# Kernel optimization log

Measured on AMD Instinct MI355X. Metric: run time of the kernel, lower is better.

The kernel has to match this reference:

```python
import jax, jax.numpy as jnp
import numpy as np

N_HEADS = 16
HEAD_DIM = 64
SEQ_LEN = 2048
BATCH = 1


def alibi_slopes(n_heads):
    start = 2.0 ** (-8.0 / n_heads)
    return jnp.asarray([start * start ** i for i in range(n_heads)], dtype=jnp.float32)


def setup_inputs() -> dict:
    key = jax.random.key(0)
    kq, kk, kv = jax.random.split(key, 3)
    shape = (BATCH, N_HEADS, SEQ_LEN, HEAD_DIM)
    return {
        "q": jax.random.normal(kq, shape, dtype=jnp.float32),
        "k": jax.random.normal(kk, shape, dtype=jnp.float32),
        "v": jax.random.normal(kv, shape, dtype=jnp.float32),
    }


def reference(q, k, v):
    # q,k,v: [B,H,S,D]
    seq_len = q.shape[2]
    head_dim = q.shape[3]
    scale = 1.0 / np.sqrt(head_dim).astype(np.float32)
    # scores: [B,H,S,S]
    scores = jnp.einsum("bhsd,bhtd->bhst", q, k) * scale
    pos = jnp.arange(seq_len)
    # distances[i, j] = j - i  (pos.unsqueeze(0) - pos.unsqueeze(1))
    distances = (pos[None, :] - pos[:, None]).astype(jnp.float32)  # [S,S]
    slopes = alibi_slopes(q.shape[1])  # [H]
    alibi = slopes[:, None, None] * distances[None, :, :]  # [H,S,S]
    scores = scores + alibi[None]
    attn = jax.nn.softmax(scores, axis=-1)
    return jnp.einsum("bhst,bhtd->bhsd", attn, v)
```

## Files before the change

### kernel.cpp

```cpp
#include <hip/hip_runtime.h>
#include <hip/hip_bf16.h>
#include <stdint.h>
#include <math.h>

#define N_HEADS 16
#define HEAD_DIM 64
#define SEQ_LEN 2048
#define KVBLK 64
#define NT 16
#define NTILE_TOT (SEQ_LEN / 32)

typedef __bf16 bf16x8 __attribute__((ext_vector_type(8)));
typedef __bf16 bf16x4 __attribute__((ext_vector_type(4)));
typedef short  s16x4  __attribute__((ext_vector_type(4)));
typedef float  f32x4  __attribute__((ext_vector_type(4)));
typedef unsigned int u32x4 __attribute__((ext_vector_type(4)));

#if __has_builtin(__builtin_amdgcn_mfma_f32_16x16x16bf16_1k)
#define HAVE_MFMA16 1
#else
#define HAVE_MFMA16 0
#endif

#if __has_builtin(__builtin_amdgcn_global_load_lds)
#define HAVE_GLL 1
#define GLL16(gsrc, ldst)                                                     \
    __builtin_amdgcn_global_load_lds(                                         \
        (const __attribute__((address_space(1))) void*)(gsrc),                \
        (__attribute__((address_space(3))) void*)(ldst), 16, 0, 0)
#else
#define HAVE_GLL 0
#endif

static __device__ __forceinline__ unsigned pkbf(float a, float b) {
    union { __bf16 h[2]; unsigned u; } t;
    t.h[0] = (__bf16)a; t.h[1] = (__bf16)b;
    return t.u;
}

static __device__ __forceinline__ int vpos(int k) {
#if HAVE_MFMA16
    return ((k & 12) << 2) + ((k & 16) >> 1) + ((k & 3) << 1);
#else
    return k * 2;
#endif
}

__global__ __launch_bounds__(256)
void prep_kernel(const float* __restrict__ k,
                 const float* __restrict__ v,
                 char* __restrict__ kimg,
                 char* __restrict__ vtimg,
                 float* __restrict__ tilemax) {
    const int ts  = blockIdx.x;
    const int h   = blockIdx.y;
    const int tid = threadIdx.x;
    const int s0  = ts * 32;
    const size_t blk = ((size_t)h * NTILE_TOT + ts) * 4096;

    __shared__ float redmax[4];

    const int krow = tid >> 3;
    const int kcol = (tid & 7) * 8;
    const float* ks = k + ((size_t)h * SEQ_LEN + s0 + krow) * HEAD_DIM + kcol;
    f32x4 a = *(const f32x4*)ks;
    f32x4 b = *(const f32x4*)(ks + 4);
    bf16x8 kb;
    float pn = 0.0f;
    #pragma unroll
    for (int i = 0; i < 4; ++i) {
        kb[i] = (__bf16)a[i]; kb[4 + i] = (__bf16)b[i];
        pn += a[i] * a[i] + b[i] * b[i];
    }
    *(bf16x8*)(kimg + blk + krow * 128 + ((kcol * 2) ^ ((krow & 7) << 4))) = kb;

    pn += __shfl_xor(pn, 1);
    pn += __shfl_xor(pn, 2);
    pn += __shfl_xor(pn, 4);
    float wmax = pn;
    wmax = fmaxf(wmax, __shfl_xor(wmax, 8));
    wmax = fmaxf(wmax, __shfl_xor(wmax, 16));
    wmax = fmaxf(wmax, __shfl_xor(wmax, 32));
    if ((tid & 63) == 0) redmax[tid >> 6] = wmax;

    const int vc = tid & 63;
    const int vr = (tid >> 6) * 8;
    const float* vs = v + ((size_t)h * SEQ_LEN + s0 + vr) * HEAD_DIM + vc;
    bf16x4 vb0, vb1;
    #pragma unroll
    for (int j = 0; j < 4; ++j) {
        vb0[j] = (__bf16)vs[(size_t)j * HEAD_DIM];
        vb1[j] = (__bf16)vs[(size_t)(4 + j) * HEAD_DIM];
    }
    const int swzV = (vc & 7) << 4;
    *(bf16x4*)(vtimg + blk + ((vc * 64 + vpos(vr))     ^ swzV)) = vb0;
    *(bf16x4*)(vtimg + blk + ((vc * 64 + vpos(vr + 4)) ^ swzV)) = vb1;

    __syncthreads();
    if (tid == 0) {
        tilemax[h * NTILE_TOT + ts] = fmaxf(fmaxf(redmax[0], redmax[1]),
                                            fmaxf(redmax[2], redmax[3]));
    }
}

template <bool IMG>
__global__ __launch_bounds__(512, 2)
void attn_alibi_kernel(const float* __restrict__ q,
                       const float* __restrict__ k,
                       const float* __restrict__ v,
                       float* __restrict__ out,
                       const char* __restrict__ kimg,
                       const char* __restrict__ vtimg,
                       const float* __restrict__ tilemax) {
    const int tid  = threadIdx.x;
    const int wave = tid >> 6;
    const int lane = tid & 63;
    const int col  = lane & 15;
    const int g    = lane >> 4;
    const int half = wave >> 2;
    const int w4   = wave & 3;

    const int h      = blockIdx.y;
    const int qbase  = blockIdx.x * 64 + w4 * 16;
    const int kstart = half * (NT * KVBLK);

    const float* qh = q + (size_t)h * SEQ_LEN * HEAD_DIM;
    const float* kh = k + (size_t)h * SEQ_LEN * HEAD_DIM;
    const float* vh = v + (size_t)h * SEQ_LEN * HEAD_DIM;

    __shared__ alignas(16) char smem[65536];
    char* kbase  = smem + half * 16384;
    char* vtbase = smem + 32768 + half * 16384;

    const float LOG2E  = 1.4426950408889634f;
    const float scale2 = 0.125f * LOG2E;
    const float slope  = exp2f(-0.5f * (float)(h + 1));
    const float slope2 = slope * LOG2E;

    bf16x8 qf[2];
    float qn2 = 0.0f;
    {
        const float* qr = qh + (size_t)(qbase + col) * HEAD_DIM + g * 8;
        #pragma unroll
        for (int c = 0; c < 2; ++c)
            #pragma unroll
            for (int b = 0; b < 8; ++b) {
                float x = qr[c * 32 + b];
                qn2 += x * x;
                qf[c][b] = (__bf16)x;
            }
    }
    qn2 += __shfl_xor(qn2, 16);
    qn2 += __shfl_xor(qn2, 32);

    float knmax;
    if constexpr (IMG) {
        float tm = tilemax[h * NTILE_TOT + lane];
        tm = fmaxf(tm, __shfl_xor(tm, 1));
        tm = fmaxf(tm, __shfl_xor(tm, 2));
        tm = fmaxf(tm, __shfl_xor(tm, 4));
        tm = fmaxf(tm, __shfl_xor(tm, 8));
        tm = fmaxf(tm, __shfl_xor(tm, 16));
        tm = fmaxf(tm, __shfl_xor(tm, 32));
        knmax = sqrtf(tm);
    } else {
        knmax = 16.0f;
    }
    const int   kend = kstart + NT * KVBLK;
    const float m = slope2 * (float)(kend - 1 - (qbase + col))
                  + scale2 * sqrtf(qn2) * knmax * 1.05f;

    float cbm[4][4];
    #pragma unroll
    for (int i = 0; i < 4; ++i)
        #pragma unroll
        for (int r = 0; r < 4; ++r)
            cbm[i][r] = slope2 * (float)(i * 16 + g * 4 + r - (qbase + col)) - m;

    float l = 0.0f;
    f32x4 acc[4];
    #pragma unroll
    for (int dt = 0; dt < 4; ++dt) acc[dt] = (f32x4)0.0f;

    const int hid  = tid & 255;
    const int krow = hid >> 3;
    const int kcol = (hid & 7) * 8;
    const int vc   = hid & 63;
    const int vr   = (hid >> 6) * 8;

    const char* kis = nullptr; const char* vis = nullptr;
    const float* ksrc = nullptr; const float* vsrc = nullptr;
    char* kdst = nullptr; char* vtdst0 = nullptr; char* vtdst1 = nullptr;
    if constexpr (IMG) {
        const size_t base = ((size_t)h * NTILE_TOT + half * (NTILE_TOT / 2)) * 4096
                          + hid * 16;
        kis = kimg + base;  vis = vtimg + base;
#if HAVE_GLL
        kdst   = kbase + w4 * 1024;
        vtdst0 = vtbase + w4 * 1024;
#else
        kdst   = kbase + hid * 16;
        vtdst0 = vtbase + hid * 16;
#endif
    } else {
        ksrc  = kh + (size_t)(kstart + krow) * HEAD_DIM + kcol;
        kdst  = kbase + krow * 128 + ((kcol * 2) ^ ((krow & 7) << 4));
        vsrc  = vh + (size_t)(kstart + vr) * HEAD_DIM + vc;
        const int swzV = (vc & 7) << 4;
        vtdst0 = vtbase + ((vc * 64 + vpos(vr))     ^ swzV);
        vtdst1 = vtbase + ((vc * 64 + vpos(vr + 4)) ^ swzV);
    }

    f32x4 kreg[2], vreg[2];
    f32x4 kr[2][2];
    float vv[2][8];

    if constexpr (IMG) {
#if HAVE_GLL
        #pragma unroll
        for (int sb = 0; sb < 2; ++sb) {
            GLL16(kis + sb * 4096, kdst   + sb * 4096);
            GLL16(vis + sb * 4096, vtdst0 + sb * 4096);
        }
#else
        #pragma unroll
        for (int sb = 0; sb < 2; ++sb) {
            kreg[sb] = *(const f32x4*)(kis + sb * 4096);
            vreg[sb] = *(const f32x4*)(vis + sb * 4096);
            *(f32x4*)(kdst   + sb * 4096) = kreg[sb];
            *(f32x4*)(vtdst0 + sb * 4096) = vreg[sb];
        }
#endif
    } else {
        #pragma unroll
        for (int sb = 0; sb < 2; ++sb) {
            const float* ks = ksrc + (size_t)(sb * 32) * HEAD_DIM;
            const float* vs = vsrc + (size_t)(sb * 32) * HEAD_DIM;
            kr[sb][0] = *(const f32x4*)(ks);
            kr[sb][1] = *(const f32x4*)(ks + 4);
            #pragma unroll
            for (int j = 0; j < 8; ++j) vv[sb][j] = vs[(size_t)j * HEAD_DIM];
            bf16x8 kb16;
            bf16x4 vb0, vb1;
            #pragma unroll
            for (int b = 0; b < 4; ++b) {
                kb16[b] = (__bf16)kr[sb][0][b]; kb16[4 + b] = (__bf16)kr[sb][1][b];
                vb0[b] = (__bf16)vv[sb][b];     vb1[b] = (__bf16)vv[sb][4 + b];
            }
            *(bf16x8*)(kdst   + sb * 4096) = kb16;
            *(bf16x4*)(vtdst0 + sb * 4096) = vb0;
            *(bf16x4*)(vtdst1 + sb * 4096) = vb1;
        }
    }
    __syncthreads();

    for (int t = 0; t < NT; ++t) {
        const int kb  = kstart + t * KVBLK;
        const int buf = t & 1;
        const char* kbuf  = kbase + buf * 8192;
        const char* vtbuf = vtbase + buf * 8192;

#if HAVE_GLL
        if (IMG && t + 1 < NT) {
            const int nb = (t + 1) & 1;
            #pragma unroll
            for (int sb = 0; sb < 2; ++sb) {
                GLL16(kis + (size_t)((t + 1) * 2 + sb) * 4096,
                      kdst + nb * 8192 + sb * 4096);
                GLL16(vis + (size_t)((t + 1) * 2 + sb) * 4096,
                      vtdst0 + nb * 8192 + sb * 4096);
            }
        }
#endif

        f32x4 sacc[4];
        #pragma unroll
        for (int i = 0; i < 4; ++i) sacc[i] = (f32x4)0.0f;
        __builtin_amdgcn_s_setprio(1);
        #pragma unroll
        for (int sb = 0; sb < 2; ++sb) {
            #pragma unroll
            for (int jt = 0; jt < 2; ++jt) {
                const int row = jt * 16 + col;
                const int i   = sb * 2 + jt;
                #pragma unroll
                for (int c = 0; c < 2; ++c) {
                    bf16x8 kf = *(const bf16x8*)(kbuf + sb * 4096 + row * 128
                                                 + ((c * 64 + g * 16) ^ ((row & 7) << 4)));
                    sacc[i] = __builtin_amdgcn_mfma_f32_16x16x32_bf16(kf, qf[c], sacc[i], 0, 0, 0);
                }
            }
        }
        __builtin_amdgcn_s_setprio(0);

        if (t + 1 < NT) {
            if constexpr (IMG) {
#if !HAVE_GLL
                #pragma unroll
                for (int sb = 0; sb < 2; ++sb) {
                    kreg[sb] = *(const f32x4*)(kis + (size_t)((t + 1) * 2 + sb) * 4096);
                    vreg[sb] = *(const f32x4*)(vis + (size_t)((t + 1) * 2 + sb) * 4096);
                }
#endif
            } else {
                #pragma unroll
                for (int sb = 0; sb < 2; ++sb) {
                    const float* ks = ksrc + (size_t)((t + 1) * 64 + sb * 32) * HEAD_DIM;
                    const float* vs = vsrc + (size_t)((t + 1) * 64 + sb * 32) * HEAD_DIM;
                    kr[sb][0] = *(const f32x4*)(ks);
                    kr[sb][1] = *(const f32x4*)(ks + 4);
                    #pragma unroll
                    for (int j = 0; j < 8; ++j) vv[sb][j] = vs[(size_t)j * HEAD_DIM];
                }
            }
        }

        const float skb = slope2 * (float)kb;
        float p[4][4], y = 0.0f;
        #pragma unroll
        for (int i = 0; i < 4; ++i)
            #pragma unroll
            for (int r = 0; r < 4; ++r) {
                float sv = sacc[i][r] * scale2 + (cbm[i][r] + skb);
                p[i][r] = __builtin_amdgcn_exp2f(sv);
                y += p[i][r];
            }
        l += y;

#if HAVE_MFMA16
        s16x4 pb[4];
        #pragma unroll
        for (int i = 0; i < 4; ++i) {
            bf16x4 pf;
            #pragma unroll
            for (int b = 0; b < 4; ++b) pf[b] = (__bf16)p[i][b];
            pb[i] = __builtin_bit_cast(s16x4, pf);
        }
        __builtin_amdgcn_s_setprio(1);
        #pragma unroll
        for (int dt = 0; dt < 4; ++dt) {
            const int vrow = dt * 16 + col;
            const int off  = (vrow * 64 + g * 16) ^ ((vrow & 7) << 4);
            #pragma unroll
            for (int sb = 0; sb < 2; ++sb) {
                bf16x8 vf = *(const bf16x8*)(vtbuf + sb * 4096 + off);
                bf16x4 vlo = __builtin_shufflevector(vf, vf, 0, 1, 2, 3);
                bf16x4 vhi = __builtin_shufflevector(vf, vf, 4, 5, 6, 7);
                acc[dt] = __builtin_amdgcn_mfma_f32_16x16x16bf16_1k(
                    __builtin_bit_cast(s16x4, vlo), pb[sb * 2 + 0], acc[dt], 0, 0, 0);
                acc[dt] = __builtin_amdgcn_mfma_f32_16x16x16bf16_1k(
                    __builtin_bit_cast(s16x4, vhi), pb[sb * 2 + 1], acc[dt], 0, 0, 0);
            }
        }
        __builtin_amdgcn_s_setprio(0);
#else
        #pragma unroll
        for (int sb = 0; sb < 2; ++sb) {
            unsigned pk00 = pkbf(p[sb * 2][0],     p[sb * 2][1]);
            unsigned pk01 = pkbf(p[sb * 2][2],     p[sb * 2][3]);
            unsigned pk10 = pkbf(p[sb * 2 + 1][0], p[sb * 2 + 1][1]);
            unsigned pk11 = pkbf(p[sb * 2 + 1][2], p[sb * 2 + 1][3]);
            const int srcA = col + ((g & 1) << 5);
            const int srcB = srcA + 16;
            unsigned a00 = __shfl(pk00, srcA), a01 = __shfl(pk01, srcA);
            unsigned a10 = __shfl(pk10, srcA), a11 = __shfl(pk11, srcA);
            unsigned b00 = __shfl(pk00, srcB), b01 = __shfl(pk01, srcB);
            unsigned b10 = __shfl(pk10, srcB), b11 = __shfl(pk11, srcB);
            const bool hi = g >= 2;
            u32x4 pu;
            pu[0] = hi ? a10 : a00;
            pu[1] = hi ? a11 : a01;
            pu[2] = hi ? b10 : b00;
            pu[3] = hi ? b11 : b01;
            bf16x8 pf = __builtin_bit_cast(bf16x8, pu);
            #pragma unroll
            for (int dt = 0; dt < 4; ++dt) {
                const int vrow = dt * 16 + col;
                bf16x8 vf = *(const bf16x8*)(vtbuf + sb * 4096
                                + ((vrow * 64 + g * 16) ^ ((vrow & 7) << 4)));
                acc[dt] = __builtin_amdgcn_mfma_f32_16x16x32_bf16(vf, pf, acc[dt], 0, 0, 0);
            }
        }
#endif

        if (t + 1 < NT) {
            const int nb = (t + 1) & 1;
            if constexpr (IMG) {
#if !HAVE_GLL
                #pragma unroll
                for (int sb = 0; sb < 2; ++sb) {
                    *(f32x4*)(kdst   + nb * 8192 + sb * 4096) = kreg[sb];
                    *(f32x4*)(vtdst0 + nb * 8192 + sb * 4096) = vreg[sb];
                }
#endif
            } else {
                #pragma unroll
                for (int sb = 0; sb < 2; ++sb) {
                    bf16x8 kb16;
                    bf16x4 vb0, vb1;
                    #pragma unroll
                    for (int b = 0; b < 4; ++b) {
                        kb16[b] = (__bf16)kr[sb][0][b]; kb16[4 + b] = (__bf16)kr[sb][1][b];
                        vb0[b] = (__bf16)vv[sb][b];     vb1[b] = (__bf16)vv[sb][4 + b];
                    }
                    *(bf16x8*)(kdst   + nb * 8192 + sb * 4096) = kb16;
                    *(bf16x4*)(vtdst0 + nb * 8192 + sb * 4096) = vb0;
                    *(bf16x4*)(vtdst1 + nb * 8192 + sb * 4096) = vb1;
                }
            }
        }
        __syncthreads();
    }

    l += __shfl_xor(l, 16);
    l += __shfl_xor(l, 32);

    float* eacc = (float*)smem;
    float* eml  = (float*)(smem + 16384);

    if (half == 1) {
        #pragma unroll
        for (int dt = 0; dt < 4; ++dt)
            *(f32x4*)(eacc + w4 * 1024 + col * 64 + dt * 16 + g * 4) = acc[dt];
        if (g == 0) {
            eml[(w4 * 16 + col) * 2 + 0] = m;
            eml[(w4 * 16 + col) * 2 + 1] = l;
        }
    }
    __syncthreads();
    if (half == 0) {
        float m2 = eml[(w4 * 16 + col) * 2 + 0];
        float l2 = eml[(w4 * 16 + col) * 2 + 1];
        float mm = fmaxf(m, m2);
        float a1 = __builtin_amdgcn_exp2f(m - mm);
        float a2 = __builtin_amdgcn_exp2f(m2 - mm);
        float inv = 1.0f / (l * a1 + l2 * a2);
        float* orow = out + ((size_t)h * SEQ_LEN + qbase + col) * HEAD_DIM;
        #pragma unroll
        for (int dt = 0; dt < 4; ++dt) {
            f32x4 o2 = *(const f32x4*)(eacc + w4 * 1024 + col * 64 + dt * 16 + g * 4);
            *(f32x4*)(orow + dt * 16 + g * 4) = (acc[dt] * a1 + o2 * a2) * inv;
        }
    }
}

extern "C" void kernel_launch(void* const* d_in, const int* in_sizes, int n_in,
                              void* d_out, int out_size, void* d_ws, size_t ws_size,
                              hipStream_t stream) {
    const float* q = (const float*)d_in[0];
    const float* k = (const float*)d_in[1];
    const float* v = (const float*)d_in[2];
    float* out = (float*)d_out;

    const size_t imgBytes = (size_t)N_HEADS * NTILE_TOT * 4096;
    const size_t need = 2 * imgBytes + N_HEADS * NTILE_TOT * sizeof(float);

    dim3 grid(SEQ_LEN / 64, N_HEADS, 1);
    if (ws_size >= need) {
        char* kimg     = (char*)d_ws;
        char* vtimg    = kimg + imgBytes;
        float* tilemax = (float*)(vtimg + imgBytes);
        prep_kernel<<<dim3(NTILE_TOT, N_HEADS, 1), dim3(256, 1, 1), 0, stream>>>(
            k, v, kimg, vtimg, tilemax);
        attn_alibi_kernel<true><<<grid, dim3(512, 1, 1), 0, stream>>>(
            q, k, v, out, kimg, vtimg, tilemax);
    } else {
        attn_alibi_kernel<false><<<grid, dim3(512, 1, 1), 0, stream>>>(
            q, k, v, out, nullptr, nullptr, nullptr);
    }
}
```

Baseline: 43.39 us.

## Split KV four ways with 32x32 MFMA and skip ALiBi-negligible key tiles

Restructures the attention kernel so each block's eight waves split the key range into four quarters of 512 keys. Each wave handles 32 queries using 32x32 bf16 MFMAs, and the four partial results are merged through shared memory at the end. Key tiles far enough from the sequence end that the ALiBi bias drives exp2 below about 2^-160 relative to the running bound are skipped per head, which removes much of the work for steep-slope heads. The softmax scale is folded into Q, the V image layout is simplified, and launch bounds are raised to target more blocks per CU. The costs are uneven load across quarters, a four-way merge epilogue, and reliance on the precomputed max bound for the tile-skip rule to stay correct.

```diff
diff --git a/kernel.cpp b/kernel.cpp
--- a/kernel.cpp
+++ b/kernel.cpp
@@ -6,20 +6,19 @@
 #define N_HEADS 16
 #define HEAD_DIM 64
 #define SEQ_LEN 2048
-#define KVBLK 64
-#define NT 16
-#define NTILE_TOT (SEQ_LEN / 32)
+#define NTILE_TOT 64
+#define NTQ 16
 
 typedef __bf16 bf16x8 __attribute__((ext_vector_type(8)));
 typedef __bf16 bf16x4 __attribute__((ext_vector_type(4)));
 typedef short  s16x4  __attribute__((ext_vector_type(4)));
 typedef float  f32x4  __attribute__((ext_vector_type(4)));
-typedef unsigned int u32x4 __attribute__((ext_vector_type(4)));
-
-#if __has_builtin(__builtin_amdgcn_mfma_f32_16x16x16bf16_1k)
-#define HAVE_MFMA16 1
+typedef float  f32x16 __attribute__((ext_vector_type(16)));
+
+#if __has_builtin(__builtin_amdgcn_mfma_f32_32x32x8bf16_1k)
+#define HAVE_K8 1
 #else
-#define HAVE_MFMA16 0
+#define HAVE_K8 0
 #endif
 
 #if __has_builtin(__builtin_amdgcn_global_load_lds)
@@ -36,14 +35,6 @@
     union { __bf16 h[2]; unsigned u; } t;
     t.h[0] = (__bf16)a; t.h[1] = (__bf16)b;
     return t.u;
-}
-
-static __device__ __forceinline__ int vpos(int k) {
-#if HAVE_MFMA16
-    return ((k & 12) << 2) + ((k & 16) >> 1) + ((k & 3) << 1);
-#else
-    return k * 2;
-#endif
 }
 
 __global__ __launch_bounds__(256)
@@ -86,15 +77,10 @@
     const int vc = tid & 63;
     const int vr = (tid >> 6) * 8;
     const float* vs = v + ((size_t)h * SEQ_LEN + s0 + vr) * HEAD_DIM + vc;
-    bf16x4 vb0, vb1;
+    bf16x8 vb;
     #pragma unroll
-    for (int j = 0; j < 4; ++j) {
-        vb0[j] = (__bf16)vs[(size_t)j * HEAD_DIM];
-        vb1[j] = (__bf16)vs[(size_t)(4 + j) * HEAD_DIM];
-    }
-    const int swzV = (vc & 7) << 4;
-    *(bf16x4*)(vtimg + blk + ((vc * 64 + vpos(vr))     ^ swzV)) = vb0;
-    *(bf16x4*)(vtimg + blk + ((vc * 64 + vpos(vr + 4)) ^ swzV)) = vb1;
+    for (int j = 0; j < 8; ++j) vb[j] = (__bf16)vs[(size_t)j * HEAD_DIM];
+    *(bf16x8*)(vtimg + blk + ((vc * 64 + vr * 2) ^ ((vc & 7) << 4))) = vb;
 
     __syncthreads();
     if (tid == 0) {
@@ -104,7 +90,7 @@
 }
 
 template <bool IMG>
-__global__ __launch_bounds__(512, 2)
+__global__ __launch_bounds__(512, 4)
 void attn_alibi_kernel(const float* __restrict__ q,
                        const float* __restrict__ k,
                        const float* __restrict__ v,
@@ -115,42 +101,42 @@
     const int tid  = threadIdx.x;
     const int wave = tid >> 6;
     const int lane = tid & 63;
-    const int col  = lane & 15;
-    const int g    = lane >> 4;
-    const int half = wave >> 2;
-    const int w4   = wave & 3;
-
-    const int h      = blockIdx.y;
-    const int qbase  = blockIdx.x * 64 + w4 * 16;
-    const int kstart = half * (NT * KVBLK);
+    const int q5   = lane & 31;
+    const int hi   = lane >> 5;
+    const int qtr  = wave >> 1;
+    const int G    = wave & 1;
+
+    const int h     = blockIdx.y;
+    const int qbase = blockIdx.x * 64;
+    const int qpos  = qbase + G * 32 + q5;
+    const int kstart = qtr * 512;
 
     const float* qh = q + (size_t)h * SEQ_LEN * HEAD_DIM;
     const float* kh = k + (size_t)h * SEQ_LEN * HEAD_DIM;
     const float* vh = v + (size_t)h * SEQ_LEN * HEAD_DIM;
 
     __shared__ alignas(16) char smem[65536];
-    char* kbase  = smem + half * 16384;
-    char* vtbase = smem + 32768 + half * 16384;
+    char* kq = smem + qtr * 8192;
+    char* vq = smem + 32768 + qtr * 8192;
 
     const float LOG2E  = 1.4426950408889634f;
     const float scale2 = 0.125f * LOG2E;
     const float slope  = exp2f(-0.5f * (float)(h + 1));
     const float slope2 = slope * LOG2E;
 
-    bf16x8 qf[2];
+    bf16x8 qf[4];
     float qn2 = 0.0f;
     {
-        const float* qr = qh + (size_t)(qbase + col) * HEAD_DIM + g * 8;
+        const float* qr = qh + (size_t)qpos * HEAD_DIM;
         #pragma unroll
-        for (int c = 0; c < 2; ++c)
+        for (int c = 0; c < 4; ++c)
             #pragma unroll
             for (int b = 0; b < 8; ++b) {
-                float x = qr[c * 32 + b];
+                float x = qr[c * 16 + hi * 8 + b];
                 qn2 += x * x;
-                qf[c][b] = (__bf16)x;
-            }
-    }
-    qn2 += __shfl_xor(qn2, 16);
+                qf[c][b] = (__bf16)(x * scale2);
+            }
+    }
     qn2 += __shfl_xor(qn2, 32);
 
     float knmax;
@@ -166,280 +152,262 @@
     } else {
         knmax = 16.0f;
     }
-    const int   kend = kstart + NT * KVBLK;
-    const float m = slope2 * (float)(kend - 1 - (qbase + col))
+    const float m = slope2 * (float)(SEQ_LEN - 1 - qpos)
                   + scale2 * sqrtf(qn2) * knmax * 1.05f;
 
-    float cbm[4][4];
-    #pragma unroll
-    for (int i = 0; i < 4; ++i)
-        #pragma unroll
-        for (int r = 0; r < 4; ++r)
-            cbm[i][r] = slope2 * (float)(i * 16 + g * 4 + r - (qbase + col)) - m;
+    const float lim = 160.0f / (slope2 * 32.0f);
+    const int Sg   = max(0, (int)ceilf(63.0f - lim));
+    const int Sl   = min(NTQ, max(0, Sg - qtr * NTQ));
+    const int tmin = max(0, Sg - 3 * NTQ);
+
+    const float baseH = slope2 * ((float)(kstart - qpos) + 4.0f * (float)hi) - m;
+    const float s2x8  = slope2 * 8.0f;
 
     float l = 0.0f;
-    f32x4 acc[4];
-    #pragma unroll
-    for (int dt = 0; dt < 4; ++dt) acc[dt] = (f32x4)0.0f;
-
-    const int hid  = tid & 255;
-    const int krow = hid >> 3;
-    const int kcol = (hid & 7) * 8;
-    const int vc   = hid & 63;
-    const int vr   = (hid >> 6) * 8;
+    f32x16 accA = (f32x16)0.0f;
+    f32x16 accB = (f32x16)0.0f;
 
     const char* kis = nullptr; const char* vis = nullptr;
-    const float* ksrc = nullptr; const float* vsrc = nullptr;
-    char* kdst = nullptr; char* vtdst0 = nullptr; char* vtdst1 = nullptr;
+    char* kdstu = nullptr; char* vdstu = nullptr;
     if constexpr (IMG) {
-        const size_t base = ((size_t)h * NTILE_TOT + half * (NTILE_TOT / 2)) * 4096
-                          + hid * 16;
-        kis = kimg + base;  vis = vtimg + base;
-#if HAVE_GLL
-        kdst   = kbase + w4 * 1024;
-        vtdst0 = vtbase + w4 * 1024;
-#else
-        kdst   = kbase + hid * 16;
-        vtdst0 = vtbase + hid * 16;
-#endif
-    } else {
-        ksrc  = kh + (size_t)(kstart + krow) * HEAD_DIM + kcol;
-        kdst  = kbase + krow * 128 + ((kcol * 2) ^ ((krow & 7) << 4));
-        vsrc  = vh + (size_t)(kstart + vr) * HEAD_DIM + vc;
-        const int swzV = (vc & 7) << 4;
-        vtdst0 = vtbase + ((vc * 64 + vpos(vr))     ^ swzV);
-        vtdst1 = vtbase + ((vc * 64 + vpos(vr + 4)) ^ swzV);
-    }
-
-    f32x4 kreg[2], vreg[2];
-    f32x4 kr[2][2];
-    float vv[2][8];
+        const size_t blk0 = ((size_t)h * NTILE_TOT + qtr * NTQ) * 4096;
+        kis = kimg + blk0 + G * 2048 + lane * 16;
+        vis = vtimg + blk0 + G * 2048 + lane * 16;
+        kdstu = kq + G * 2048;
+        vdstu = vq + G * 2048;
+    }
 
     if constexpr (IMG) {
 #if HAVE_GLL
+        if (Sl < NTQ) {
+            const int b0 = Sl & 1;
+            #pragma unroll
+            for (int sub = 0; sub < 2; ++sub) {
+                GLL16(kis + (size_t)Sl * 4096 + sub * 1024, kdstu + b0 * 4096 + sub * 1024);
+                GLL16(vis + (size_t)Sl * 4096 + sub * 1024, vdstu + b0 * 4096 + sub * 1024);
+            }
+        }
+#else
+        if (Sl < NTQ) {
+            const int b0 = Sl & 1;
+            #pragma unroll
+            for (int sub = 0; sub < 2; ++sub) {
+                f32x4 kr = *(const f32x4*)(kis + (size_t)Sl * 4096 + sub * 1024);
+                f32x4 vr = *(const f32x4*)(vis + (size_t)Sl * 4096 + sub * 1024);
+                *(f32x4*)(kdstu + b0 * 4096 + sub * 1024 + lane * 16) = kr;
+                *(f32x4*)(vdstu + b0 * 4096 + sub * 1024 + lane * 16) = vr;
+            }
+        }
+#endif
+    }
+    __syncthreads();
+
+    for (int t = tmin; t < NTQ; ++t) {
+        const bool act = (t >= Sl);
+        const int buf  = t & 1;
+
+        if constexpr (IMG) {
+#if HAVE_GLL
+            if (act && t + 1 < NTQ) {
+                const int nb = (t + 1) & 1;
+                #pragma unroll
+                for (int sub = 0; sub < 2; ++sub) {
+                    GLL16(kis + (size_t)(t + 1) * 4096 + sub * 1024,
+                          kdstu + nb * 4096 + sub * 1024);
+                    GLL16(vis + (size_t)(t + 1) * 4096 + sub * 1024,
+                          vdstu + nb * 4096 + sub * 1024);
+                }
+            }
+#else
+            if (act && t + 1 < NTQ) {
+                const int nb = (t + 1) & 1;
+                #pragma unroll
+                for (int sub = 0; sub < 2; ++sub) {
+                    f32x4 kr = *(const f32x4*)(kis + (size_t)(t + 1) * 4096 + sub * 1024);
+                    f32x4 vr = *(const f32x4*)(vis + (size_t)(t + 1) * 4096 + sub * 1024);
+                    *(f32x4*)(kdstu + nb * 4096 + sub * 1024 + lane * 16) = kr;
+                    *(f32x4*)(vdstu + nb * 4096 + sub * 1024 + lane * 16) = vr;
+                }
+            }
+#endif
+        } else {
+            if (act) {
+                const int qt = tid & 127;
+                const int s0 = kstart + t * 32;
+                const int krow = qt >> 2, c4 = qt & 3;
+                const float* ks = kh + (size_t)(s0 + krow) * HEAD_DIM + c4 * 16;
+                bf16x8 kb0, kb1;
+                #pragma unroll
+                for (int i = 0; i < 8; ++i) { kb0[i] = (__bf16)ks[i]; kb1[i] = (__bf16)ks[8 + i]; }
+                const int swk = (krow & 7) << 4;
+                char* kd = kq + buf * 4096 + krow * 128;
+                *(bf16x8*)(kd + ((c4 * 32) ^ swk))      = kb0;
+                *(bf16x8*)(kd + ((c4 * 32 + 16) ^ swk)) = kb1;
+
+                const int vc = qt & 63, vg = qt >> 6;
+                const float* vs = vh + (size_t)(s0 + vg * 16) * HEAD_DIM + vc;
+                bf16x8 v0, v1;
+                #pragma unroll
+                for (int j = 0; j < 8; ++j) {
+                    v0[j] = (__bf16)vs[(size_t)j * HEAD_DIM];
+                    v1[j] = (__bf16)vs[(size_t)(8 + j) * HEAD_DIM];
+                }
+                const int swv = (vc & 7) << 4;
+                char* vd = vq + buf * 4096;
+                *(bf16x8*)(vd + ((vc * 64 + vg * 32) ^ swv))      = v0;
+                *(bf16x8*)(vd + ((vc * 64 + vg * 32 + 16) ^ swv)) = v1;
+            }
+            __syncthreads();
+        }
+
+        if (act) {
+            const char* kbuf = kq + buf * 4096;
+            f32x16 sacc = (f32x16)0.0f;
+            __builtin_amdgcn_s_setprio(1);
+            #pragma unroll
+            for (int dt2 = 0; dt2 < 4; ++dt2) {
+                bf16x8 kf = *(const bf16x8*)(kbuf + q5 * 128
+                                             + ((dt2 * 32 + hi * 16) ^ ((q5 & 7) << 4)));
+                sacc = __builtin_amdgcn_mfma_f32_32x32x16_bf16(kf, qf[dt2], sacc, 0, 0, 0);
+            }
+            __builtin_amdgcn_s_setprio(0);
+
+            const float bt0 = baseH + slope2 * (float)(32 * t);
+            float p[16], y = 0.0f;
+            #pragma unroll
+            for (int u = 0; u < 4; ++u) {
+                const float bt = bt0 + s2x8 * (float)u;
+                #pragma unroll
+                for (int j = 0; j < 4; ++j) {
+                    float sv = sacc[u * 4 + j] + (bt + slope2 * (float)j);
+                    p[u * 4 + j] = __builtin_amdgcn_exp2f(sv);
+                    y += p[u * 4 + j];
+                }
+            }
+            l += y;
+
+            const char* vbuf = vq + buf * 4096;
+#if HAVE_K8
+            s16x4 pb[4];
+            #pragma unroll
+            for (int j = 0; j < 4; ++j) {
+                bf16x4 pf;
+                #pragma unroll
+                for (int b = 0; b < 4; ++b) pf[b] = (__bf16)p[j * 4 + b];
+                pb[j] = __builtin_bit_cast(s16x4, pf);
+            }
+            __builtin_amdgcn_s_setprio(1);
+            #pragma unroll
+            for (int j = 0; j < 4; ++j) {
+                {
+                    const int d = q5;
+                    bf16x4 vf = *(const bf16x4*)(vbuf
+                        + ((d * 64 + 16 * j + 8 * hi) ^ ((d & 7) << 4)));
+                    accA = __builtin_amdgcn_mfma_f32_32x32x8bf16_1k(
+                        __builtin_bit_cast(s16x4, vf), pb[j], accA, 0, 0, 0);
+                }
+                {
+                    const int d = 32 + q5;
+                    bf16x4 vf = *(const bf16x4*)(vbuf
+                        + ((d * 64 + 16 * j + 8 * hi) ^ ((d & 7) << 4)));
+                    accB = __builtin_amdgcn_mfma_f32_32x32x8bf16_1k(
+                        __builtin_bit_cast(s16x4, vf), pb[j], accB, 0, 0, 0);
+                }
+            }
+            __builtin_amdgcn_s_setprio(0);
+#else
+            unsigned own[4], own2[4], sw[4], sw2[4];
+            #pragma unroll
+            for (int u = 0; u < 4; ++u) {
+                own[u]  = pkbf(p[4 * u + 0], p[4 * u + 1]);
+                own2[u] = pkbf(p[4 * u + 2], p[4 * u + 3]);
+                sw[u]   = __shfl_xor(own[u], 32);
+                sw2[u]  = __shfl_xor(own2[u], 32);
+            }
+            __builtin_amdgcn_s_setprio(1);
+            #pragma unroll
+            for (int ko8 = 0; ko8 < 4; ko8 += 2) {
+                unsigned w0 = hi ? sw[ko8 + 1]  : own[ko8];
+                unsigned w1 = hi ? sw2[ko8 + 1] : own2[ko8];
+                unsigned w2 = hi ? own[ko8 + 1] : sw[ko8];
+                unsigned w3 = hi ? own2[ko8 + 1]: sw2[ko8];
+                unsigned uarr[4] = {w0, w1, w2, w3};
+                bf16x8 pf8;
+                #pragma unroll
+                for (int i = 0; i < 4; ++i) {
+                    pf8[2 * i]     = __builtin_bit_cast(bf16x4, (unsigned long long)0)[0];
+                }
+                union { unsigned u[4]; bf16x8 v; } cvt;
+                cvt.u[0] = w0; cvt.u[1] = w1; cvt.u[2] = w2; cvt.u[3] = w3;
+                pf8 = cvt.v;
+                #pragma unroll
+                for (int dt = 0; dt < 2; ++dt) {
+                    const int d = dt * 32 + q5;
+                    bf16x8 vf = *(const bf16x8*)(vbuf
+                        + ((d * 64 + ko8 * 16 + 16 * hi) ^ ((d & 7) << 4)));
+                    if (dt == 0)
+                        accA = __builtin_amdgcn_mfma_f32_32x32x16_bf16(vf, pf8, accA, 0, 0, 0);
+                    else
+                        accB = __builtin_amdgcn_mfma_f32_32x32x16_bf16(vf, pf8, accB, 0, 0, 0);
+                }
+            }
+            __builtin_amdgcn_s_setprio(0);
+#endif
+        }
+        __syncthreads();
+    }
+
+    l += __shfl_xor(l, 32);
+
+    float* eacc = (float*)smem;
+    float* eml  = (float*)(smem + 49152);
+
+    if (qtr != 0) {
+        float* ea = eacc + (size_t)(qtr - 1) * 4096 + (G * 32 + q5) * 64;
         #pragma unroll
-        for (int sb = 0; sb < 2; ++sb) {
-            GLL16(kis + sb * 4096, kdst   + sb * 4096);
-            GLL16(vis + sb * 4096, vtdst0 + sb * 4096);
-        }
-#else
+        for (int u = 0; u < 4; ++u) {
+            f32x4 sa = {accA[4 * u], accA[4 * u + 1], accA[4 * u + 2], accA[4 * u + 3]};
+            f32x4 sb = {accB[4 * u], accB[4 * u + 1], accB[4 * u + 2], accB[4 * u + 3]};
+            *(f32x4*)(ea + 8 * u + 4 * hi)      = sa;
+            *(f32x4*)(ea + 32 + 8 * u + 4 * hi) = sb;
+        }
+        if (hi == 0) {
+            eml[((qtr - 1) * 64 + G * 32 + q5) * 2 + 0] = m;
+            eml[((qtr - 1) * 64 + G * 32 + q5) * 2 + 1] = l;
+        }
+    }
+    __syncthreads();
+    if (qtr == 0) {
+        float mm = m, mi[3], li[3];
         #pragma unroll
-        for (int sb = 0; sb < 2; ++sb) {
-            kreg[sb] = *(const f32x4*)(kis + sb * 4096);
-            vreg[sb] = *(const f32x4*)(vis + sb * 4096);
-            *(f32x4*)(kdst   + sb * 4096) = kreg[sb];
-            *(f32x4*)(vtdst0 + sb * 4096) = vreg[sb];
-        }
-#endif
-    } else {
+        for (int i = 0; i < 3; ++i) {
+            mi[i] = eml[(i * 64 + G * 32 + q5) * 2 + 0];
+            li[i] = eml[(i * 64 + G * 32 + q5) * 2 + 1];
+            mm = fmaxf(mm, mi[i]);
+        }
+        float a0 = __builtin_amdgcn_exp2f(m - mm);
+        float lt = l * a0;
+        float ai[3];
         #pragma unroll
-        for (int sb = 0; sb < 2; ++sb) {
-            const float* ks = ksrc + (size_t)(sb * 32) * HEAD_DIM;
-            const float* vs = vsrc + (size_t)(sb * 32) * HEAD_DIM;
-            kr[sb][0] = *(const f32x4*)(ks);
-            kr[sb][1] = *(const f32x4*)(ks + 4);
-            #pragma unroll
-            for (int j = 0; j < 8; ++j) vv[sb][j] = vs[(size_t)j * HEAD_DIM];
-            bf16x8 kb16;
-            bf16x4 vb0, vb1;
-            #pragma unroll
-            for (int b = 0; b < 4; ++b) {
-                kb16[b] = (__bf16)kr[sb][0][b]; kb16[4 + b] = (__bf16)kr[sb][1][b];
-                vb0[b] = (__bf16)vv[sb][b];     vb1[b] = (__bf16)vv[sb][4 + b];
-            }
-            *(bf16x8*)(kdst   + sb * 4096) = kb16;
-            *(bf16x4*)(vtdst0 + sb * 4096) = vb0;
-            *(bf16x4*)(vtdst1 + sb * 4096) = vb1;
-        }
-    }
-    __syncthreads();
-
-    for (int t = 0; t < NT; ++t) {
-        const int kb  = kstart + t * KVBLK;
-        const int buf = t & 1;
-        const char* kbuf  = kbase + buf * 8192;
-        const char* vtbuf = vtbase + buf * 8192;
-
-#if HAVE_GLL
-        if (IMG && t + 1 < NT) {
-            const int nb = (t + 1) & 1;
-            #pragma unroll
-            for (int sb = 0; sb < 2; ++sb) {
-                GLL16(kis + (size_t)((t + 1) * 2 + sb) * 4096,
-                      kdst + nb * 8192 + sb * 4096);
-                GLL16(vis + (size_t)((t + 1) * 2 + sb) * 4096,
-                      vtdst0 + nb * 8192 + sb * 4096);
-            }
-        }
-#endif
-
-        f32x4 sacc[4];
+        for (int i = 0; i < 3; ++i) {
+            ai[i] = __builtin_amdgcn_exp2f(mi[i] - mm);
+            lt += li[i] * ai[i];
+        }
+        const float inv = 1.0f / lt;
+        float* orow = out + ((size_t)h * SEQ_LEN + qbase + G * 32 + q5) * HEAD_DIM;
         #pragma unroll
-        for (int i = 0; i < 4; ++i) sacc[i] = (f32x4)0.0f;
-        __builtin_amdgcn_s_setprio(1);
-        #pragma unroll
-        for (int sb = 0; sb < 2; ++sb) {
-            #pragma unroll
-            for (int jt = 0; jt < 2; ++jt) {
-                const int row = jt * 16 + col;
-                const int i   = sb * 2 + jt;
-                #pragma unroll
-                for (int c = 0; c < 2; ++c) {
-                    bf16x8 kf = *(const bf16x8*)(kbuf + sb * 4096 + row * 128
-                                                 + ((c * 64 + g * 16) ^ ((row & 7) << 4)));
-                    sacc[i] = __builtin_amdgcn_mfma_f32_16x16x32_bf16(kf, qf[c], sacc[i], 0, 0, 0);
-                }
-            }
-        }
-        __builtin_amdgcn_s_setprio(0);
-
-        if (t + 1 < NT) {
-            if constexpr (IMG) {
-#if !HAVE_GLL
-                #pragma unroll
-                for (int sb = 0; sb < 2; ++sb) {
-                    kreg[sb] = *(const f32x4*)(kis + (size_t)((t + 1) * 2 + sb) * 4096);
-                    vreg[sb] = *(const f32x4*)(vis + (size_t)((t + 1) * 2 + sb) * 4096);
-                }
-#endif
-            } else {
-                #pragma unroll
-                for (int sb = 0; sb < 2; ++sb) {
-                    const float* ks = ksrc + (size_t)((t + 1) * 64 + sb * 32) * HEAD_DIM;
-                    const float* vs = vsrc + (size_t)((t + 1) * 64 + sb * 32) * HEAD_DIM;
-                    kr[sb][0] = *(const f32x4*)(ks);
-                    kr[sb][1] = *(const f32x4*)(ks + 4);
-                    #pragma unroll
-                    for (int j = 0; j < 8; ++j) vv[sb][j] = vs[(size_t)j * HEAD_DIM];
-                }
-            }
-        }
-
-        const float skb = slope2 * (float)kb;
-        float p[4][4], y = 0.0f;
-        #pragma unroll
-        for (int i = 0; i < 4; ++i)
-            #pragma unroll
-            for (int r = 0; r < 4; ++r) {
-                float sv = sacc[i][r] * scale2 + (cbm[i][r] + skb);
-                p[i][r] = __builtin_amdgcn_exp2f(sv);
-                y += p[i][r];
-            }
-        l += y;
-
-#if HAVE_MFMA16
-        s16x4 pb[4];
-        #pragma unroll
-        for (int i = 0; i < 4; ++i) {
-            bf16x4 pf;
-            #pragma unroll
-            for (int b = 0; b < 4; ++b) pf[b] = (__bf16)p[i][b];
-            pb[i] = __builtin_bit_cast(s16x4, pf);
-        }
-        __builtin_amdgcn_s_setprio(1);
-        #pragma unroll
-        for (int dt = 0; dt < 4; ++dt) {
-            const int vrow = dt * 16 + col;
-            const int off  = (vrow * 64 + g * 16) ^ ((vrow & 7) << 4);
-            #pragma unroll
-            for (int sb = 0; sb < 2; ++sb) {
-                bf16x8 vf = *(const bf16x8*)(vtbuf + sb * 4096 + off);
-                bf16x4 vlo = __builtin_shufflevector(vf, vf, 0, 1, 2, 3);
-                bf16x4 vhi = __builtin_shufflevector(vf, vf, 4, 5, 6, 7);
-                acc[dt] = __builtin_amdgcn_mfma_f32_16x16x16bf16_1k(
-                    __builtin_bit_cast(s16x4, vlo), pb[sb * 2 + 0], acc[dt], 0, 0, 0);
-                acc[dt] = __builtin_amdgcn_mfma_f32_16x16x16bf16_1k(
-                    __builtin_bit_cast(s16x4, vhi), pb[sb * 2 + 1], acc[dt], 0, 0, 0);
-            }
-        }
-        __builtin_amdgcn_s_setprio(0);
-#else
-        #pragma unroll
-        for (int sb = 0; sb < 2; ++sb) {
-            unsigned pk00 = pkbf(p[sb * 2][0],     p[sb * 2][1]);
-            unsigned pk01 = pkbf(p[sb * 2][2],     p[sb * 2][3]);
-            unsigned pk10 = pkbf(p[sb * 2 + 1][0], p[sb * 2 + 1][1]);
-            unsigned pk11 = pkbf(p[sb * 2 + 1][2], p[sb * 2 + 1][3]);
-            const int srcA = col + ((g & 1) << 5);
-            const int srcB = srcA + 16;
-            unsigned a00 = __shfl(pk00, srcA), a01 = __shfl(pk01, srcA);
-            unsigned a10 = __shfl(pk10, srcA), a11 = __shfl(pk11, srcA);
-            unsigned b00 = __shfl(pk00, srcB), b01 = __shfl(pk01, srcB);
-            unsigned b10 = __shfl(pk10, srcB), b11 = __shfl(pk11, srcB);
-            const bool hi = g >= 2;
-            u32x4 pu;
-            pu[0] = hi ? a10 : a00;
-            pu[1] = hi ? a11 : a01;
-            pu[2] = hi ? b10 : b00;
-            pu[3] = hi ? b11 : b01;
-            bf16x8 pf = __builtin_bit_cast(bf16x8, pu);
-            #pragma unroll
-            for (int dt = 0; dt < 4; ++dt) {
-                const int vrow = dt * 16 + col;
-                bf16x8 vf = *(const bf16x8*)(vtbuf + sb * 4096
-                                + ((vrow * 64 + g * 16) ^ ((vrow & 7) << 4)));
-                acc[dt] = __builtin_amdgcn_mfma_f32_16x16x32_bf16(vf, pf, acc[dt], 0, 0, 0);
-            }
-        }
-#endif
-
-        if (t + 1 < NT) {
-            const int nb = (t + 1) & 1;
-            if constexpr (IMG) {
-#if !HAVE_GLL
-                #pragma unroll
-                for (int sb = 0; sb < 2; ++sb) {
-                    *(f32x4*)(kdst   + nb * 8192 + sb * 4096) = kreg[sb];
-                    *(f32x4*)(vtdst0 + nb * 8192 + sb * 4096) = vreg[sb];
-                }
-#endif
-            } else {
-                #pragma unroll
-                for (int sb = 0; sb < 2; ++sb) {
-                    bf16x8 kb16;
-                    bf16x4 vb0, vb1;
-                    #pragma unroll
-                    for (int b = 0; b < 4; ++b) {
-                        kb16[b] = (__bf16)kr[sb][0][b]; kb16[4 + b] = (__bf16)kr[sb][1][b];
-                        vb0[b] = (__bf16)vv[sb][b];     vb1[b] = (__bf16)vv[sb][4 + b];
-                    }
-                    *(bf16x8*)(kdst   + nb * 8192 + sb * 4096) = kb16;
-                    *(bf16x4*)(vtdst0 + nb * 8192 + sb * 4096) = vb0;
-                    *(bf16x4*)(vtdst1 + nb * 8192 + sb * 4096) = vb1;
-                }
-            }
-        }
-        __syncthreads();
-    }
-
-    l += __shfl_xor(l, 16);
-    l += __shfl_xor(l, 32);
-
-    float* eacc = (float*)smem;
-    float* eml  = (float*)(smem + 16384);
-
-    if (half == 1) {
-        #pragma unroll
-        for (int dt = 0; dt < 4; ++dt)
-            *(f32x4*)(eacc + w4 * 1024 + col * 64 + dt * 16 + g * 4) = acc[dt];
-        if (g == 0) {
-            eml[(w4 * 16 + col) * 2 + 0] = m;
-            eml[(w4 * 16 + col) * 2 + 1] = l;
-        }
-    }
-    __syncthreads();
-    if (half == 0) {
-        float m2 = eml[(w4 * 16 + col) * 2 + 0];
-        float l2 = eml[(w4 * 16 + col) * 2 + 1];
-        float mm = fmaxf(m, m2);
-        float a1 = __builtin_amdgcn_exp2f(m - mm);
-        float a2 = __builtin_amdgcn_exp2f(m2 - mm);
-        float inv = 1.0f / (l * a1 + l2 * a2);
-        float* orow = out + ((size_t)h * SEQ_LEN + qbase + col) * HEAD_DIM;
-        #pragma unroll
-        for (int dt = 0; dt < 4; ++dt) {
-            f32x4 o2 = *(const f32x4*)(eacc + w4 * 1024 + col * 64 + dt * 16 + g * 4);
-            *(f32x4*)(orow + dt * 16 + g * 4) = (acc[dt] * a1 + o2 * a2) * inv;
+        for (int u = 0; u < 4; ++u) {
+            f32x4 oa = {accA[4 * u], accA[4 * u + 1], accA[4 * u + 2], accA[4 * u + 3]};
+            f32x4 ob = {accB[4 * u], accB[4 * u + 1], accB[4 * u + 2], accB[4 * u + 3]};
+            oa *= a0; ob *= a0;
+            #pragma unroll
+            for (int i = 0; i < 3; ++i) {
+                const float* ea = eacc + (size_t)i * 4096 + (G * 32 + q5) * 64;
+                oa += *(const f32x4*)(ea + 8 * u + 4 * hi) * ai[i];
+                ob += *(const f32x4*)(ea + 32 + 8 * u + 4 * hi) * ai[i];
+            }
+            *(f32x4*)(orow + 8 * u + 4 * hi)      = oa * inv;
+            *(f32x4*)(orow + 32 + 8 * u + 4 * hi) = ob * inv;
         }
     }
 }
```

New measurement: 46.76 us, median of 3. +7.8%, slower.
